# Performance work log

Hardware: AMD Instinct MI355X
Metric: run time of the kernel (lower is better)

Reference implementation:

```python
import jax, jax.numpy as jnp
import numpy as np

SEQ_LEN = 2048
EMBED = 1024
HIDDEN = 1024
BATCH = 4


def setup_inputs() -> dict:
    key = jax.random.key(0)
    ks = jax.random.split(key, 7)
    # xavier_uniform for weights: limit = sqrt(6/(fan_in+fan_out))
    lim = float(np.sqrt(6.0 / (EMBED + HIDDEN)))
    blim = float(1.0 / np.sqrt(EMBED))  # torch Linear default bias init U(-1/sqrt(fan_in), ...)
    inputs = jax.random.normal(ks[0], (BATCH, SEQ_LEN, EMBED), dtype=jnp.float32)
    Wq = jax.random.uniform(ks[1], (HIDDEN, EMBED), jnp.float32, -lim, lim)
    Wk = jax.random.uniform(ks[2], (HIDDEN, EMBED), jnp.float32, -lim, lim)
    Wv = jax.random.uniform(ks[3], (HIDDEN, EMBED), jnp.float32, -lim, lim)
    bq = jax.random.uniform(ks[4], (HIDDEN,), jnp.float32, -blim, blim)
    bk = jax.random.uniform(ks[5], (HIDDEN,), jnp.float32, -blim, blim)
    bv = jax.random.uniform(ks[6], (HIDDEN,), jnp.float32, -blim, blim)
    return {"inputs": inputs, "Wq": Wq, "bq": bq, "Wk": Wk, "bk": bk, "Wv": Wv, "bv": bv}


def reference(inputs, Wq, bq, Wk, bk, Wv, bv):
    B, S, E = inputs.shape
    q = jnp.einsum('bse,he->bsh', inputs, Wq) + bq  # [B,S,H]
    k = jnp.einsum('bse,he->bsh', inputs, Wk) + bk
    v = jnp.einsum('bse,he->bsh', inputs, Wv) + bv
    # NOTE: source scales by 1/sqrt(embed_size), not hidden_size
    scores = jnp.einsum('bqh,bkh->bqk', q, k) / jnp.sqrt(jnp.float32(E))
    causal = jnp.tril(jnp.ones((S, S), dtype=bool))  # [S,S]
    scores = jnp.where(causal[None, :, :], scores, -jnp.inf)
    attn = jax.nn.softmax(scores, axis=-1)
    return jnp.einsum('bqk,bkh->bqh', attn, v)
```

## Files before the change

### kernel.cpp

```cpp
#include <hip/hip_runtime.h>
#include <cstdint>
#include <cstddef>
#include <math.h>

typedef unsigned short u16;

#define S_LEN 2048
#define EMB   1024
#define HID   1024
#define NB    4

using bf16x8 = __attribute__((ext_vector_type(8))) __bf16;
using f32x4  = __attribute__((ext_vector_type(4))) float;


__device__ __forceinline__ u16 f2bf(float f) {
  union { float f; uint32_t u; } c; c.f = f;
  uint32_t u = c.u;
  uint32_t r = (u + 0x7fffu + ((u >> 16) & 1u)) >> 16;
  return (u16)r;
}

__device__ __forceinline__ void gld_lds16(const u16* g, u16* l) {
  auto gp = (const __attribute__((address_space(1))) uint32_t*)(uintptr_t)(const void*)g;
  auto lp = (__attribute__((address_space(3))) uint32_t*)(uintptr_t)(void*)l;
  __builtin_amdgcn_global_load_lds(gp, lp, 16, 0, 0);
}


__global__ void cvt_f32_bf16(const float* __restrict__ in, u16* __restrict__ out, int n4) {
  int i = blockIdx.x * blockDim.x + threadIdx.x;
  int stride = gridDim.x * blockDim.x;
  for (; i < n4; i += stride) {
    float4 v = reinterpret_cast<const float4*>(in)[i];
    reinterpret_cast<ushort4*>(out)[i] =
      make_ushort4(f2bf(v.x), f2bf(v.y), f2bf(v.z), f2bf(v.w));
  }
}

__global__ void cvt3_f32_bf16(const float* __restrict__ a, const float* __restrict__ b,
                              const float* __restrict__ c, u16* __restrict__ out, int n4) {
  const float* src = (blockIdx.y == 0) ? a : (blockIdx.y == 1) ? b : c;
  u16* dst = out + (size_t)blockIdx.y * (size_t)n4 * 4;
  int i = blockIdx.x * blockDim.x + threadIdx.x;
  int stride = gridDim.x * blockDim.x;
  for (; i < n4; i += stride) {
    float4 v = reinterpret_cast<const float4*>(src)[i];
    reinterpret_cast<ushort4*>(dst)[i] =
      make_ushort4(f2bf(v.x), f2bf(v.y), f2bf(v.z), f2bf(v.w));
  }
}


template<int EPI>
__global__ __launch_bounds__(512, 2)
void gemm4p(const u16* __restrict__ A, const u16* __restrict__ Bw, void* __restrict__ Cv,
            const float* __restrict__ b0, const float* __restrict__ b1,
            const float* __restrict__ b2, u16* __restrict__ VT,
            int N, int K, long sA, long sB, long sC, float scale)
{
  const int z = blockIdx.z;
  A  += (long)z * sA;
  Bw += (long)z * sB;

  __shared__ __align__(16) u16 smem[49152];

  const int tid = threadIdx.x;
  const int l   = tid & 63;
  const int w   = tid >> 6;
  const int wr  = w >> 2;
  const int wc  = w & 3;

  const int nwg = gridDim.x * gridDim.y;
  const int lin = blockIdx.y * gridDim.x + blockIdx.x;
  const int sw  = (lin & 7) * (nwg >> 3) + (lin >> 3);
  const int bm  = (sw / gridDim.x) * 128;
  const int bn  = (sw % gridDim.x) * 256;

  int kend = K;
  if constexpr (EPI == 3) kend = bm + 128;
  const int NTILE = kend >> 6;

  const int arow = w * 16 + (l >> 2);
  const int acs  = (l & 3) ^ (((l >> 5) & 1) << 1);
  const u16* gbA  = A  + (long)(bm + arow) * K + acs * 8;
  const u16* gbB  = Bw + (long)(bn + arow) * K + acs * 8;
  const u16* gbB2 = gbB + 128L * K;

#define STGH(t, s, dbase)                                                       \
  do {                                                                          \
    const long _o = (long)(t) * 64 + (s) * 32;                                  \
    gld_lds16(gbA  + _o, smem + (dbase) + (s) * 4096 + w * 512);                \
    gld_lds16(gbB  + _o, smem + (dbase) + 8192 + (s) * 8192 + w * 512);         \
    gld_lds16(gbB2 + _o, smem + (dbase) + 8192 + (s) * 8192 + 4096 + w * 512);  \
  } while (0)

  const int lr  = l & 15;
  const int kg  = l >> 4;
  const int kgp = kg ^ (((lr >> 3) & 1) << 1);
  int aoff[4], boff[4];
#pragma unroll
  for (int m = 0; m < 4; ++m) aoff[m] = (wr * 64 + m * 16 + lr) * 32 + kgp * 8;
#pragma unroll
  for (int n = 0; n < 4; ++n) boff[n] = (wc * 64 + n * 16 + lr) * 32 + kgp * 8;

  f32x4 acc[4][4] = {};

  STGH(0, 0, 0);
  STGH(0, 1, 0);
  asm volatile("s_waitcnt vmcnt(0)" ::: "memory");
  __builtin_amdgcn_s_barrier();
  asm volatile("" ::: "memory");

#define PHASE(d, s, STGSTMT)                                                    \
  do {                                                                          \
    const u16* hA = smem + (d) * 24576 + (s) * 4096;                            \
    const u16* hB = smem + (d) * 24576 + 8192 + (s) * 8192;                     \
    bf16x8 av[4], bv[4];                                                        \
    _Pragma("unroll")                                                           \
    for (int m_ = 0; m_ < 4; ++m_)                                              \
      av[m_] = *reinterpret_cast<const bf16x8*>(hA + aoff[m_]);                 \
    _Pragma("unroll")                                                           \
    for (int n_ = 0; n_ < 4; ++n_)                                              \
      bv[n_] = *reinterpret_cast<const bf16x8*>(hB + boff[n_]);                 \
    STGSTMT;                                                                    \
    asm volatile("s_waitcnt vmcnt(3)" ::: "memory");                            \
    __builtin_amdgcn_s_barrier();                                               \
    asm volatile("" ::: "memory");                                              \
    __builtin_amdgcn_s_setprio(1);                                              \
    _Pragma("unroll")                                                           \
    for (int m_ = 0; m_ < 4; ++m_)                                              \
      _Pragma("unroll")                                                         \
      for (int n_ = 0; n_ < 4; ++n_)                                            \
        acc[m_][n_] = __builtin_amdgcn_mfma_f32_16x16x32_bf16(                  \
            av[m_], bv[n_], acc[m_][n_], 0, 0, 0);                              \
    __builtin_amdgcn_s_setprio(0);                                              \
    asm volatile("" ::: "memory");                                              \
    __builtin_amdgcn_s_barrier();                                               \
    asm volatile("" ::: "memory");                                              \
  } while (0)

#pragma unroll 1
  for (int i = 0; i < NTILE / 2; ++i) {
    const int t1 = 2 * i + 1;
    const int t2 = (2 * i + 2 < NTILE) ? 2 * i + 2 : NTILE - 1;
    PHASE(0, 0, STGH(t1, 0, 24576));
    PHASE(0, 1, STGH(t1, 1, 24576));
    PHASE(1, 0, STGH(t2, 0, 0));
    PHASE(1, 1, STGH(t2, 1, 0));
  }
#undef PHASE
#undef STGH

  if constexpr (EPI == 3) {
    float* C = (float*)Cv + (long)z * sC;
#pragma unroll
    for (int n = 0; n < 4; ++n) {
      const int col = bn + wc * 64 + n * 16 + lr;
#pragma unroll
      for (int m = 0; m < 4; ++m) {
        const int row0 = bm + wr * 64 + m * 16 + kg * 4;
#pragma unroll
        for (int q = 0; q < 4; ++q)
          C[(long)(row0 + q) * N + col] = acc[m][n][q];
      }
    }
  } else {
    constexpr long M = (long)NB * S_LEN;
    const int sel = bn >> 10;
    const float* bias = (sel == 0) ? b0 : (sel == 1) ? b1 : b2;
    u16* QK = (u16*)Cv;
#pragma unroll
    for (int n = 0; n < 4; ++n) {
      const int col = bn + wc * 64 + n * 16 + lr;
      const int h   = col & (HID - 1);
      const float bbv = bias[h];
#pragma unroll
      for (int m = 0; m < 4; ++m) {
        const int row0 = bm + wr * 64 + m * 16 + kg * 4;
        if (sel < 2) {
          u16* dst = QK + (long)sel * M * HID + (long)row0 * HID + h;
#pragma unroll
          for (int q = 0; q < 4; ++q)
            dst[(long)q * HID] = f2bf(acc[m][n][q] + bbv);
        } else {
          const int b = row0 >> 11;
          const int s = row0 & (S_LEN - 1);
          ushort4 o = make_ushort4(f2bf(acc[m][n][0] + bbv), f2bf(acc[m][n][1] + bbv),
                                   f2bf(acc[m][n][2] + bbv), f2bf(acc[m][n][3] + bbv));
          *reinterpret_cast<ushort4*>(VT + ((long)b * HID + h) * S_LEN + s) = o;
        }
      }
    }
  }
}


#define BM 128
#define BN 128
#define BK 32

__global__ __launch_bounds__(256)
void gemm_bt2(const u16* __restrict__ A, const u16* __restrict__ B, float* __restrict__ Cv,
              int N, int K, long sA, long sB, long sC, float scale)
{
  const int z = blockIdx.z;
  A += (long)z * sA;
  B += (long)z * sB;

  __shared__ __align__(16) u16 As[BM * BK];
  __shared__ __align__(16) u16 Bs[BN * BK];

  const int t    = threadIdx.x;
  const int lane = t & 63;
  const int wave = t >> 6;
  const int wr   = wave >> 1, wc = wave & 1;

  const int x0 = blockIdx.x;
  const int x  = (x0 & 7) * ((int)gridDim.x >> 3) + (x0 >> 3);
  int bi = (int)((sqrtf(8.0f * (float)x + 1.0f) - 1.0f) * 0.5f);
  while ((bi + 1) * (bi + 2) / 2 <= x) ++bi;
  while (bi * (bi + 1) / 2 > x) --bi;
  const int bm = bi * BM;
  const int bn = (x - bi * (bi + 1) / 2) * BN;

  f32x4 acc[4][4] = {};

  const int r  = t >> 2, c8 = (t & 3) * 8;
  const u16* gA = A + (long)(bm + r) * K + c8;
  const u16* gB = B + (long)(bn + r) * K + c8;
  u16* sA0 = As + wave * 512;
  u16* sB0 = Bs + wave * 512;

  const int lr = lane & 15;
  const int kg = lane >> 4;
  const int aoff = (wr * 64 + lr) * BK + kg * 8;
  const int boff = (wc * 64 + lr) * BK + kg * 8;

  for (int kt = 0; kt < K; kt += BK) {
    gld_lds16(gA,                sA0);
    gld_lds16(gA + 64 * (long)K, sA0 + 2048);
    gld_lds16(gB,                sB0);
    gld_lds16(gB + 64 * (long)K, sB0 + 2048);
    gA += BK; gB += BK;
    __syncthreads();

    bf16x8 af[4], bf[4];
#pragma unroll
    for (int i = 0; i < 4; ++i)
      af[i] = *reinterpret_cast<const bf16x8*>(&As[aoff + i * 16 * BK]);
#pragma unroll
    for (int j = 0; j < 4; ++j)
      bf[j] = *reinterpret_cast<const bf16x8*>(&Bs[boff + j * 16 * BK]);
#pragma unroll
    for (int i = 0; i < 4; ++i)
#pragma unroll
      for (int j = 0; j < 4; ++j)
        acc[i][j] = __builtin_amdgcn_mfma_f32_16x16x32_bf16(af[i], bf[j], acc[i][j], 0, 0, 0);
    __syncthreads();
  }

  float* C = Cv + (long)z * sC;
#pragma unroll
  for (int j = 0; j < 4; ++j) {
    const int col = bn + wc * 64 + j * 16 + lr;
#pragma unroll
    for (int i = 0; i < 4; ++i) {
      const int row0 = bm + wr * 64 + i * 16 + kg * 4;
#pragma unroll
      for (int q = 0; q < 4; ++q) {
        const int row = row0 + q;
        float v = acc[i][j][q] * scale;
        if (col > row) v = -1e30f;
        C[(long)row * N + col] = v;
      }
    }
  }
}


__global__ __launch_bounds__(256)
void softmax_causal(const float* __restrict__ Sc, u16* __restrict__ P, long sS, long sP)
{
  const int row  = blockIdx.x;
  const int z    = blockIdx.y;
  const int kend = ((row >> 7) + 1) << 7;
  const float* srow = Sc + (long)z * sS + (long)row * S_LEN;
  u16*        prow = P  + (long)z * sP + (long)row * S_LEN;
  const int t = threadIdx.x;
  const int lane = t & 63, wave = t >> 6;

  const bool p0 = (4 * t) < kend;
  const bool p1 = (1024 + 4 * t) < kend;

  float4 v0 = make_float4(-1e30f, -1e30f, -1e30f, -1e30f);
  float4 v1 = v0;
  if (p0) v0 = reinterpret_cast<const float4*>(srow)[t];
  if (p1) v1 = reinterpret_cast<const float4*>(srow)[t + 256];

  float mx = fmaxf(fmaxf(fmaxf(v0.x, v0.y), fmaxf(v0.z, v0.w)),
                   fmaxf(fmaxf(v1.x, v1.y), fmaxf(v1.z, v1.w)));

  __shared__ float red[8];
#pragma unroll
  for (int off = 32; off; off >>= 1) mx = fmaxf(mx, __shfl_down(mx, off));
  if (lane == 0) red[wave] = mx;
  __syncthreads();
  mx = fmaxf(fmaxf(red[0], red[1]), fmaxf(red[2], red[3]));

  float e[8];
  e[0] = __expf(v0.x - mx); e[1] = __expf(v0.y - mx);
  e[2] = __expf(v0.z - mx); e[3] = __expf(v0.w - mx);
  e[4] = __expf(v1.x - mx); e[5] = __expf(v1.y - mx);
  e[6] = __expf(v1.z - mx); e[7] = __expf(v1.w - mx);

  float sm = ((e[0] + e[1]) + (e[2] + e[3])) + ((e[4] + e[5]) + (e[6] + e[7]));
#pragma unroll
  for (int off = 32; off; off >>= 1) sm += __shfl_down(sm, off);
  if (lane == 0) red[4 + wave] = sm;
  __syncthreads();
  sm = (red[4] + red[5]) + (red[6] + red[7]);

  const float inv = 1.0f / sm;
  if (p0)
    reinterpret_cast<ushort4*>(prow)[t] =
      make_ushort4(f2bf(e[0]*inv), f2bf(e[1]*inv), f2bf(e[2]*inv), f2bf(e[3]*inv));
  if (p1)
    reinterpret_cast<ushort4*>(prow)[t + 256] =
      make_ushort4(f2bf(e[4]*inv), f2bf(e[5]*inv), f2bf(e[6]*inv), f2bf(e[7]*inv));
}


extern "C" void kernel_launch(void* const* d_in, const int* in_sizes, int n_in,
                              void* d_out, int out_size, void* d_ws, size_t ws_size,
                              hipStream_t stream)
{
  const float* x  = (const float*)d_in[0];
  const float* Wq = (const float*)d_in[1];
  const float* bq = (const float*)d_in[2];
  const float* Wk = (const float*)d_in[3];
  const float* bk = (const float*)d_in[4];
  const float* Wv = (const float*)d_in[5];
  const float* bv = (const float*)d_in[6];
  float* out = (float*)d_out;

  const long M = (long)NB * S_LEN;

  u16* xb  = (u16*)d_ws;
  u16* wqb = xb  + M * EMB;
  u16* Qb  = wqb + 3L * HID * EMB;
  u16* Kb  = Qb  + M * HID;
  u16* VT  = Kb  + M * HID;
  char* rest = (char*)(VT + M * HID);
  const size_t used  = (size_t)(rest - (char*)d_ws);
  const size_t ssz   = (size_t)S_LEN * S_LEN;
  const size_t need4 = used + (size_t)NB * ssz * 4 + (size_t)NB * ssz * 2;
  const int nb = (ws_size >= need4) ? NB : 1;
  float* scores = (float*)rest;
  u16*   P      = (u16*)(rest + (size_t)nb * ssz * 4);

  cvt_f32_bf16<<<2048, 256, 0, stream>>>(x, xb, (int)(M * EMB / 4));
  cvt3_f32_bf16<<<dim3(512, 3), 256, 0, stream>>>(Wq, Wk, Wv, wqb, HID * EMB / 4);

  gemm4p<4><<<dim3(12, 64, 1), 512, 0, stream>>>(xb, wqb, Qb, bq, bk, bv, VT,
                                                 3 * HID, EMB, 0, 0, 0, 1.0f);

  const float scale = 0.03125f;
  const int NTb = S_LEN / BM;
  const int TRI = NTb * (NTb + 1) / 2;

  if (nb == NB) {
    dim3 gs(TRI, 1, NB);
    gemm_bt2<<<gs, 256, 0, stream>>>(Qb, Kb, scores, S_LEN, HID,
                                     (long)S_LEN * HID, (long)S_LEN * HID, (long)ssz, scale);
    softmax_causal<<<dim3(S_LEN, NB), 256, 0, stream>>>(scores, P, (long)ssz, (long)ssz);
    gemm4p<3><<<dim3(HID / 256, S_LEN / 128, NB), 512, 0, stream>>>(
        P, VT, out, nullptr, nullptr, nullptr, nullptr,
        HID, S_LEN, (long)ssz, (long)HID * S_LEN, (long)S_LEN * HID, 1.0f);
  } else {
    for (int b = 0; b < NB; ++b) {
      const u16* Qbb = Qb + (long)b * S_LEN * HID;
      const u16* Kbb = Kb + (long)b * S_LEN * HID;
      const u16* VTb = VT + (long)b * HID * S_LEN;
      float* outb = out + (long)b * S_LEN * HID;
      dim3 gs(TRI, 1, 1);
      gemm_bt2<<<gs, 256, 0, stream>>>(Qbb, Kbb, scores, S_LEN, HID, 0, 0, 0, scale);
      softmax_causal<<<dim3(S_LEN, 1), 256, 0, stream>>>(scores, P, 0, 0);
      gemm4p<3><<<dim3(HID / 256, S_LEN / 128, 1), 512, 0, stream>>>(
          P, VTb, outb, nullptr, nullptr, nullptr, nullptr,
          HID, S_LEN, 0, 0, 0, 1.0f);
    }
  }
}
```

Baseline: 190.7 us.

## Add causal-aware PV GEMM with paired row blocks and drop trailing barrier

```diff
diff --git a/kernel.cpp b/kernel.cpp
--- a/kernel.cpp
+++ b/kernel.cpp
@@ -136,8 +136,6 @@
             av[m_], bv[n_], acc[m_][n_], 0, 0, 0);                              \
     __builtin_amdgcn_s_setprio(0);                                              \
     asm volatile("" ::: "memory");                                              \
-    __builtin_amdgcn_s_barrier();                                               \
-    asm volatile("" ::: "memory");                                              \
   } while (0)
 
 #pragma unroll 1
@@ -190,6 +188,118 @@
                                    f2bf(acc[m][n][2] + bbv), f2bf(acc[m][n][3] + bbv));
           *reinterpret_cast<ushort4*>(VT + ((long)b * HID + h) * S_LEN + s) = o;
         }
+      }
+    }
+  }
+}
+
+
+__global__ __launch_bounds__(512, 2)
+void gemm_pv(const u16* __restrict__ Pm, const u16* __restrict__ VTm, float* __restrict__ Cm)
+{
+  const int z = blockIdx.z;
+  const u16* A = Pm  + (long)z * S_LEN * S_LEN;
+  const u16* B = VTm + (long)z * HID * S_LEN;
+  float*    Cz = Cm  + (long)z * S_LEN * HID;
+
+  __shared__ __align__(16) u16 smem[32768];
+
+  const int tid = threadIdx.x;
+  const int l   = tid & 63;
+  const int w   = tid >> 6;
+  const int wr  = w >> 2;
+  const int wc  = w & 3;
+  const int bn  = blockIdx.x * 128;
+  const int pr  = blockIdx.y;
+
+  const int lr  = l & 15;
+  const int kg  = l >> 4;
+  const int kgp = kg ^ (((lr >> 3) & 1) << 1);
+  int aoff[4], boff[2];
+#pragma unroll
+  for (int m = 0; m < 4; ++m) aoff[m] = (wr * 64 + m * 16 + lr) * 32 + kgp * 8;
+#pragma unroll
+  for (int n = 0; n < 2; ++n) boff[n] = (wc * 32 + n * 16 + lr) * 32 + kgp * 8;
+
+  const int arow = w * 16 + (l >> 2);
+  const int acs  = (l & 3) ^ (((l >> 5) & 1) << 1);
+
+#pragma unroll 1
+  for (int it = 0; it < 2; ++it) {
+    const int bi = (it == 0) ? (15 - pr) : pr;
+    const int bm = bi * 128;
+    const int NTILE = (bi + 1) * 2;
+
+    const u16* gbA = A + (long)(bm + arow) * S_LEN + acs * 8;
+    const u16* gbB = B + (long)(bn + arow) * S_LEN + acs * 8;
+
+#define STGH(t, s, dbase)                                                       \
+  do {                                                                          \
+    const long _o = (long)(t) * 64 + (s) * 32;                                  \
+    gld_lds16(gbA + _o, smem + (dbase) + (s) * 4096 + w * 512);                 \
+    gld_lds16(gbB + _o, smem + (dbase) + 8192 + (s) * 4096 + w * 512);          \
+  } while (0)
+
+    if (it) {
+      __builtin_amdgcn_s_barrier();
+      asm volatile("" ::: "memory");
+    }
+
+    f32x4 acc[4][2] = {};
+
+    STGH(0, 0, 0);
+    STGH(0, 1, 0);
+    asm volatile("s_waitcnt vmcnt(0)" ::: "memory");
+    __builtin_amdgcn_s_barrier();
+    asm volatile("" ::: "memory");
+
+#define PHASE(d, s, STGSTMT)                                                    \
+  do {                                                                          \
+    const u16* hA = smem + (d) * 16384 + (s) * 4096;                            \
+    const u16* hB = smem + (d) * 16384 + 8192 + (s) * 4096;                     \
+    bf16x8 av[4], bv[2];                                                        \
+    _Pragma("unroll")                                                           \
+    for (int m_ = 0; m_ < 4; ++m_)                                              \
+      av[m_] = *reinterpret_cast<const bf16x8*>(hA + aoff[m_]);                 \
+    _Pragma("unroll")                                                           \
+    for (int n_ = 0; n_ < 2; ++n_)                                              \
+      bv[n_] = *reinterpret_cast<const bf16x8*>(hB + boff[n_]);                 \
+    STGSTMT;                                                                    \
+    asm volatile("s_waitcnt vmcnt(2)" ::: "memory");                            \
+    __builtin_amdgcn_s_barrier();                                               \
+    asm volatile("" ::: "memory");                                              \
+    __builtin_amdgcn_s_setprio(1);                                              \
+    _Pragma("unroll")                                                           \
+    for (int m_ = 0; m_ < 4; ++m_)                                              \
+      _Pragma("unroll")                                                         \
+      for (int n_ = 0; n_ < 2; ++n_)                                            \
+        acc[m_][n_] = __builtin_amdgcn_mfma_f32_16x16x32_bf16(                  \
+            av[m_], bv[n_], acc[m_][n_], 0, 0, 0);                              \
+    __builtin_amdgcn_s_setprio(0);                                              \
+    asm volatile("" ::: "memory");                                              \
+  } while (0)
+
+#pragma unroll 1
+    for (int i = 0; i < NTILE / 2; ++i) {
+      const int t1 = 2 * i + 1;
+      const int t2 = (2 * i + 2 < NTILE) ? 2 * i + 2 : NTILE - 1;
+      PHASE(0, 0, STGH(t1, 0, 16384));
+      PHASE(0, 1, STGH(t1, 1, 16384));
+      PHASE(1, 0, STGH(t2, 0, 0));
+      PHASE(1, 1, STGH(t2, 1, 0));
+    }
+#undef PHASE
+#undef STGH
+
+#pragma unroll
+    for (int n = 0; n < 2; ++n) {
+      const int col = bn + wc * 32 + n * 16 + lr;
+#pragma unroll
+      for (int m = 0; m < 4; ++m) {
+        const int row0 = bm + wr * 64 + m * 16 + kg * 4;
+#pragma unroll
+        for (int q = 0; q < 4; ++q)
+          Cz[(long)(row0 + q) * HID + col] = acc[m][n][q];
       }
     }
   }
@@ -374,9 +484,7 @@
     gemm_bt2<<<gs, 256, 0, stream>>>(Qb, Kb, scores, S_LEN, HID,
                                      (long)S_LEN * HID, (long)S_LEN * HID, (long)ssz, scale);
     softmax_causal<<<dim3(S_LEN, NB), 256, 0, stream>>>(scores, P, (long)ssz, (long)ssz);
-    gemm4p<3><<<dim3(HID / 256, S_LEN / 128, NB), 512, 0, stream>>>(
-        P, VT, out, nullptr, nullptr, nullptr, nullptr,
-        HID, S_LEN, (long)ssz, (long)HID * S_LEN, (long)S_LEN * HID, 1.0f);
+    gemm_pv<<<dim3(8, 8, NB), 512, 0, stream>>>(P, VT, out);
   } else {
     for (int b = 0; b < NB; ++b) {
       const u16* Qbb = Qb + (long)b * S_LEN * HID;
@@ -386,9 +494,7 @@
       dim3 gs(TRI, 1, 1);
       gemm_bt2<<<gs, 256, 0, stream>>>(Qbb, Kbb, scores, S_LEN, HID, 0, 0, 0, scale);
       softmax_causal<<<dim3(S_LEN, 1), 256, 0, stream>>>(scores, P, 0, 0);
-      gemm4p<3><<<dim3(HID / 256, S_LEN / 128, 1), 512, 0, stream>>>(
-          P, VTb, outb, nullptr, nullptr, nullptr, nullptr,
-          HID, S_LEN, 0, 0, 0, 1.0f);
-    }
-  }
-}
+      gemm_pv<<<dim3(8, 8, 1), 512, 0, stream>>>(P, VTb, outb);
+    }
+  }
+}
```

Result: faster. 179.2 us (-6.0%).
